# Performance work log

Hardware: AMD Instinct MI355X
Metric: run time of the kernel (lower is better)

Reference implementation:

```python
import math
import jax, jax.numpy as jnp
import numpy as np

D_MODEL = 2048
HEAD = 128
DEPTH = 12
LAMBDA_INIT = 0.8 - 0.6 * math.exp(-0.3 * DEPTH)
RMS_EPS = float(np.finfo(np.float32).eps)  # torch RMSNorm default eps=None -> finfo.eps


def setup_inputs() -> dict:
    key = jax.random.key(0)
    ks = jax.random.split(key, 9)
    B, S = 2, 4096
    std_l = 0.1
    return {
        "x": jax.random.normal(ks[0], (B, S, D_MODEL), dtype=jnp.float32),
        "Wq": jax.random.normal(ks[1], (HEAD, D_MODEL), dtype=jnp.float32) / math.sqrt(D_MODEL),
        "Wk": jax.random.normal(ks[2], (HEAD, D_MODEL), dtype=jnp.float32) / math.sqrt(D_MODEL),
        "Wv": jax.random.normal(ks[3], (HEAD, D_MODEL), dtype=jnp.float32) / math.sqrt(D_MODEL),
        "lambda_q1": std_l * jax.random.normal(ks[4], (HEAD // 2,), dtype=jnp.float32),
        "lambda_q2": std_l * jax.random.normal(ks[5], (HEAD // 2,), dtype=jnp.float32),
        "lambda_k1": std_l * jax.random.normal(ks[6], (HEAD // 2,), dtype=jnp.float32),
        "lambda_k2": std_l * jax.random.normal(ks[7], (HEAD // 2,), dtype=jnp.float32),
        "rms_weight": jnp.ones((HEAD,), dtype=jnp.float32),
    }


def reference(x, Wq, Wk, Wv, lambda_q1, lambda_q2, lambda_k1, lambda_k2, rms_weight):
    # projections (torch Linear: x @ W.T)
    q = jnp.einsum("bsd,hd->bsh", x, Wq)
    k = jnp.einsum("bsd,hd->bsh", x, Wk)
    v = jnp.einsum("bsd,hd->bsh", x, Wv)
    h2 = HEAD // 2
    q1, q2 = q[..., :h2], q[..., h2:]
    k1, k2 = k[..., :h2], k[..., h2:]
    scale = 1.0 / math.sqrt(h2)
    attn1 = jax.nn.softmax(jnp.einsum("bqh,bkh->bqk", q1, k1) * scale, axis=-1)
    attn2 = jax.nn.softmax(jnp.einsum("bqh,bkh->bqk", q2, k2) * scale, axis=-1)
    lam = jnp.exp(jnp.dot(lambda_q1, lambda_k1)) - jnp.exp(jnp.dot(lambda_q2, lambda_k2)) + LAMBDA_INIT
    attn_out = jnp.einsum("bqk,bkh->bqh", attn1 - lam * attn2, v)
    # RMSNorm over last dim
    rms = jax.lax.rsqrt(jnp.mean(attn_out * attn_out, axis=-1, keepdims=True) + RMS_EPS)
    return (1.0 - LAMBDA_INIT) * (attn_out * rms * rms_weight)
```

## Files before the change

kernel.cpp:

```cpp
#include <hip/hip_runtime.h>
#include <hip/hip_bf16.h>
#include <math.h>

#define S_LEN 4096
#define DMODEL 2048
#define HEADD 128

typedef __attribute__((ext_vector_type(8))) short short8;
typedef __attribute__((ext_vector_type(4))) float floatx4;

__device__ __forceinline__ short f2bs(float f) {
  __hip_bfloat16 h = __float2bfloat16(f);
  short s; __builtin_memcpy(&s, &h, 2); return s;
}
__device__ __forceinline__ float bs2f(short s) {
  unsigned u = ((unsigned)(unsigned short)s) << 16;
  float f; __builtin_memcpy(&f, &u, 4); return f;
}
__device__ __forceinline__ int pkbf(float a, float b) {
  return (int)(((unsigned)(unsigned short)f2bs(b) << 16) |
               (unsigned)(unsigned short)f2bs(a));
}
__device__ __forceinline__ float fexp2(float x) { return __builtin_amdgcn_exp2f(x); }

__global__ __launch_bounds__(256) void convw_kernel(const float* __restrict__ wq,
                                                    const float* __restrict__ wk,
                                                    const float* __restrict__ wv,
                                                    short* __restrict__ wc) {
  const int per = 128 * 2048;
  int e = (blockIdx.x * blockDim.x + threadIdx.x) * 4;
  const float* src = (e < per) ? wq : (e < 2 * per) ? wk : wv;
  int off = e & (per - 1);
  float4 v = *(const float4*)(src + off);
  short4 r;
  r.x = f2bs(v.x); r.y = f2bs(v.y); r.z = f2bs(v.z); r.w = f2bs(v.w);
  *(short4*)(wc + e) = r;
}

__global__ __launch_bounds__(256, 3) void proj_kernel(const float* __restrict__ x,
                                                      const short* __restrict__ wc,
                                                      short* __restrict__ qm,
                                                      short* __restrict__ kb,
                                                      short* __restrict__ vstage) {
  const int tid = threadIdx.x;
  const int w = tid >> 6;
  const int lane = tid & 63;
  const int lo = lane & 15, g = lane >> 4;
  const int id = blockIdx.x;
  const int nq = id >> 7, mb = id & 127;
  const int m0 = mb * 64;
  const int n0 = nq * 96;

  __shared__ short xt[2][64 * 64];
  __shared__ short wt[2][96 * 64];

  const int r8 = tid >> 3, sc = tid & 7;
  const float* xs0 = x + (size_t)(m0 + r8) * DMODEL + sc * 8;
  const float* xs1 = x + (size_t)(m0 + 32 + r8) * DMODEL + sc * 8;
  const short* ws0 = wc + (size_t)(n0 + r8) * DMODEL + sc * 8;
  const short* ws1 = wc + (size_t)(n0 + 32 + r8) * DMODEL + sc * 8;
  const short* ws2 = wc + (size_t)(n0 + 64 + r8) * DMODEL + sc * 8;
  const int xl0 = r8 * 64 + ((sc ^ (r8 & 7)) * 8);
  const int xl1 = (32 + r8) * 64 + ((sc ^ (r8 & 7)) * 8);
  const int wlo0 = r8 * 64 + ((sc ^ (r8 & 7)) * 8);
  const int wlo1 = (32 + r8) * 64 + ((sc ^ (r8 & 7)) * 8);
  const int wlo2 = (64 + r8) * 64 + ((sc ^ (r8 & 7)) * 8);

  const int mrow = (w >> 1) * 32;
  const int ncol = (w & 1) * 48;
  int aoff[2][2], boff[3][2];
#pragma unroll
  for (int mi = 0; mi < 2; ++mi) {
    int r = mrow + mi * 16 + lo;
#pragma unroll
    for (int kc = 0; kc < 2; ++kc)
      aoff[mi][kc] = r * 64 + (((kc * 4 + g) ^ (r & 7)) * 8);
  }
#pragma unroll
  for (int t = 0; t < 3; ++t) {
    int r = ncol + t * 16 + lo;
#pragma unroll
    for (int kc = 0; kc < 2; ++kc)
      boff[t][kc] = r * 64 + (((kc * 4 + g) ^ (r & 7)) * 8);
  }

  floatx4 acc[2][3];
#pragma unroll
  for (int mi = 0; mi < 2; ++mi)
#pragma unroll
    for (int t = 0; t < 3; ++t) acc[mi][t] = floatx4{0.f, 0.f, 0.f, 0.f};

  {
    float4 a0 = *(const float4*)(xs0), a1 = *(const float4*)(xs0 + 4);
    float4 b0 = *(const float4*)(xs1), b1 = *(const float4*)(xs1 + 4);
    int4 w0 = *(const int4*)(ws0);
    int4 w1 = *(const int4*)(ws1);
    int4 w2 = *(const int4*)(ws2);
    short8 sA, sB;
    sA[0]=f2bs(a0.x); sA[1]=f2bs(a0.y); sA[2]=f2bs(a0.z); sA[3]=f2bs(a0.w);
    sA[4]=f2bs(a1.x); sA[5]=f2bs(a1.y); sA[6]=f2bs(a1.z); sA[7]=f2bs(a1.w);
    sB[0]=f2bs(b0.x); sB[1]=f2bs(b0.y); sB[2]=f2bs(b0.z); sB[3]=f2bs(b0.w);
    sB[4]=f2bs(b1.x); sB[5]=f2bs(b1.y); sB[6]=f2bs(b1.z); sB[7]=f2bs(b1.w);
    *(short8*)&xt[0][xl0] = sA;
    *(short8*)&xt[0][xl1] = sB;
    *(int4*)&wt[0][wlo0] = w0;
    *(int4*)&wt[0][wlo1] = w1;
    *(int4*)&wt[0][wlo2] = w2;
  }
  __syncthreads();

  int cur = 0;
#pragma unroll 1
  for (int it = 0; it < 32; ++it) {
    float4 a0, a1, b0, b1;
    int4 w0, w1, w2;
    if (it + 1 < 32) {
      const int k = (it + 1) * 64;
      a0 = *(const float4*)(xs0 + k); a1 = *(const float4*)(xs0 + k + 4);
      b0 = *(const float4*)(xs1 + k); b1 = *(const float4*)(xs1 + k + 4);
      w0 = *(const int4*)(ws0 + k);
      w1 = *(const int4*)(ws1 + k);
      w2 = *(const int4*)(ws2 + k);
    }

    {
      const short* xb = &xt[cur][0];
      const short* wb = &wt[cur][0];
      short8 af[2][2], bf[3][2];
#pragma unroll
      for (int mi = 0; mi < 2; ++mi)
#pragma unroll
        for (int kc = 0; kc < 2; ++kc) af[mi][kc] = *(const short8*)(xb + aoff[mi][kc]);
#pragma unroll
      for (int t = 0; t < 3; ++t)
#pragma unroll
        for (int kc = 0; kc < 2; ++kc) bf[t][kc] = *(const short8*)(wb + boff[t][kc]);
#pragma unroll
      for (int kc = 0; kc < 2; ++kc)
#pragma unroll
        for (int mi = 0; mi < 2; ++mi)
#pragma unroll
          for (int t = 0; t < 3; ++t)
            acc[mi][t] = __builtin_amdgcn_mfma_f32_16x16x32_bf16(af[mi][kc], bf[t][kc], acc[mi][t], 0, 0, 0);
    }

    if (it + 1 < 32) {
      short8 sA, sB;
      sA[0]=f2bs(a0.x); sA[1]=f2bs(a0.y); sA[2]=f2bs(a0.z); sA[3]=f2bs(a0.w);
      sA[4]=f2bs(a1.x); sA[5]=f2bs(a1.y); sA[6]=f2bs(a1.z); sA[7]=f2bs(a1.w);
      sB[0]=f2bs(b0.x); sB[1]=f2bs(b0.y); sB[2]=f2bs(b0.z); sB[3]=f2bs(b0.w);
      sB[4]=f2bs(b1.x); sB[5]=f2bs(b1.y); sB[6]=f2bs(b1.z); sB[7]=f2bs(b1.w);
      *(short8*)&xt[cur ^ 1][xl0] = sA;
      *(short8*)&xt[cur ^ 1][xl1] = sB;
      *(int4*)&wt[cur ^ 1][wlo0] = w0;
      *(int4*)&wt[cur ^ 1][wlo1] = w1;
      *(int4*)&wt[cur ^ 1][wlo2] = w2;
    }
    __syncthreads();
    cur ^= 1;
  }

#pragma unroll
  for (int t = 0; t < 3; ++t) {
    int n = n0 + ncol + t * 16 + lo;
#pragma unroll
    for (int mi = 0; mi < 2; ++mi)
#pragma unroll
      for (int j = 0; j < 4; ++j) {
        int m = m0 + mrow + mi * 16 + g * 4 + j;
        float v = acc[mi][t][j];
        if (n < HEADD) {
          qm[(size_t)m * HEADD + n] = f2bs(v * 0.18033688011112042f);
        } else if (n < 2 * HEADD) {
          kb[(size_t)m * HEADD + (n - HEADD)] = f2bs(v);
        } else {
          vstage[(size_t)m * HEADD + (n - 2 * HEADD)] = f2bs(v);
        }
      }
  }
}

__global__ __launch_bounds__(256) void conv_v_kernel(const short* __restrict__ vstage,
                                                     short* __restrict__ vt) {
  const int tid = threadIdx.x;
  const int bb = blockIdx.x >> 6, st = blockIdx.x & 63;
  const int s0 = st * 64;

  __shared__ short ld[64][136];

  const int r = tid >> 2, c8 = (tid & 3) * 32;
#pragma unroll
  for (int q = 0; q < 4; ++q) {
    const size_t off = (size_t)(bb * 4096 + s0 + r) * 128 + c8 + q * 8;
    *(short8*)(&ld[r][c8 + q * 8]) = *(const short8*)(vstage + off);
  }
  __syncthreads();

  const int h = tid >> 1, sh = (tid & 1) * 32;
#pragma unroll
  for (int q = 0; q < 4; ++q) {
    short8 t;
#pragma unroll
    for (int i = 0; i < 8; ++i) t[i] = ld[sh + q * 8 + i][h];
    *(short8*)(vt + ((size_t)bb * 128 + h) * 4096 + s0 + sh + q * 8) = t;
  }
}

__global__ __launch_bounds__(256, 3) void attn_kernel(const short* __restrict__ qm,
                                                      const short* __restrict__ kb,
                                                      const short* __restrict__ vt,
                                                      short* __restrict__ po,
                                                      float* __restrict__ pls) {
  const int tid = threadIdx.x;
  const int w = tid >> 6;
  const int lane = tid & 63;
  const int lo = lane & 15, g = lane >> 4;
  const int qsp = w >> 1;
  const int s = w & 1;
  const int id = blockIdx.x;
  const int ksp = id & 7;
  const int qblk = id >> 3;
  const int b = qblk >> 6;
  const int kv_base = ksp * 512;

  __shared__ short kt[2][32 * 128];
  __shared__ short vl[2][128 * 32];

  const int kr0 = tid >> 4, kck = tid & 15;
  const int vr0 = tid >> 2, vck = tid & 3;
  const short* kS = kb + (size_t)b * S_LEN * HEADD;
  const short* vS = vt + (size_t)b * HEADD * S_LEN;
  const int kld0 = kr0 * 128 + ((kck ^ (kr0 & 7)) * 8);
  const int kld1 = (kr0 + 16) * 128 + ((kck ^ (kr0 & 7)) * 8);
  const int vld0 = vr0 * 32 + ((vck ^ (vr0 & 3)) * 8);
  const int vld1 = (vr0 + 64) * 32 + ((vck ^ (vr0 & 3)) * 8);

  const int rowqA = qblk * 64 + qsp * 32;
  const int rowqB = rowqA + 16;
  const short* qrowA = qm + (size_t)(rowqA + lo) * HEADD + s * 64;
  const short* qrowB = qm + (size_t)(rowqB + lo) * HEADD + s * 64;
  const short8 qA0 = *(const short8*)(qrowA + g * 8);
  const short8 qA1 = *(const short8*)(qrowA + 32 + g * 8);
  const short8 qB0 = *(const short8*)(qrowB + g * 8);
  const short8 qB1 = *(const short8*)(qrowB + 32 + g * 8);

  floatx4 accA[8], accB[8];
#pragma unroll
  for (int n = 0; n < 8; ++n) {
    accA[n] = floatx4{0.f, 0.f, 0.f, 0.f};
    accB[n] = floatx4{0.f, 0.f, 0.f, 0.f};
  }
  float lxA = 0.f, lxB = 0.f;

  const int kc0 = ((s * 8 + g) ^ (lo & 7)) * 8;
  const int kc1 = ((s * 8 + 4 + g) ^ (lo & 7)) * 8;
  const int kro0 = lo * 128, kro1 = (16 + lo) * 128;
  const int vco = (g ^ (lo & 3)) * 8;

  const int gA = (g & 1) * 2;
  const int idx0 = lo + 16 * gA, idx1 = idx0 + 16;
  const bool hi = (g >= 2);

  {
    int4 ka = *(const int4*)(kS + (size_t)(kv_base + kr0) * HEADD + kck * 8);
    int4 kbx = *(const int4*)(kS + (size_t)(kv_base + kr0 + 16) * HEADD + kck * 8);
    int4 va = *(const int4*)(vS + (size_t)vr0 * S_LEN + kv_base + vck * 8);
    int4 vb = *(const int4*)(vS + (size_t)(vr0 + 64) * S_LEN + kv_base + vck * 8);
    *(int4*)(&kt[0][kld0]) = ka;
    *(int4*)(&kt[0][kld1]) = kbx;
    *(int4*)(&vl[0][vld0]) = va;
    *(int4*)(&vl[0][vld1]) = vb;
  }
  __syncthreads();

  int cur = 0;
#pragma unroll 1
  for (int it = 0; it < 16; ++it) {
    int4 ka, kbx, va, vb;
    if (it + 1 < 16) {
      const int kvn = kv_base + (it + 1) * 32;
      ka  = *(const int4*)(kS + (size_t)(kvn + kr0) * HEADD + kck * 8);
      kbx = *(const int4*)(kS + (size_t)(kvn + kr0 + 16) * HEADD + kck * 8);
      va  = *(const int4*)(vS + (size_t)vr0 * S_LEN + kvn + vck * 8);
      vb  = *(const int4*)(vS + (size_t)(vr0 + 64) * S_LEN + kvn + vck * 8);
    }

    const short* kbase = &kt[cur][0];
    short8 a00 = *(const short8*)(kbase + kro0 + kc0);
    short8 a01 = *(const short8*)(kbase + kro0 + kc1);
    short8 a10 = *(const short8*)(kbase + kro1 + kc0);
    short8 a11 = *(const short8*)(kbase + kro1 + kc1);

    floatx4 z = floatx4{0.f, 0.f, 0.f, 0.f};
    floatx4 u;
    u = __builtin_amdgcn_mfma_f32_16x16x32_bf16(a00, qA0, z, 0, 0, 0);
    floatx4 T0A = __builtin_amdgcn_mfma_f32_16x16x32_bf16(a01, qA1, u, 0, 0, 0);
    u = __builtin_amdgcn_mfma_f32_16x16x32_bf16(a10, qA0, z, 0, 0, 0);
    floatx4 T1A = __builtin_amdgcn_mfma_f32_16x16x32_bf16(a11, qA1, u, 0, 0, 0);
    u = __builtin_amdgcn_mfma_f32_16x16x32_bf16(a00, qB0, z, 0, 0, 0);
    floatx4 T0B = __builtin_amdgcn_mfma_f32_16x16x32_bf16(a01, qB1, u, 0, 0, 0);
    u = __builtin_amdgcn_mfma_f32_16x16x32_bf16(a10, qB0, z, 0, 0, 0);
    floatx4 T1B = __builtin_amdgcn_mfma_f32_16x16x32_bf16(a11, qB1, u, 0, 0, 0);

    short8 paA, paB;
    {
      float p0 = fexp2(T0A[0]), p1 = fexp2(T0A[1]), p2 = fexp2(T0A[2]), p3 = fexp2(T0A[3]);
      float p4 = fexp2(T1A[0]), p5 = fexp2(T1A[1]), p6 = fexp2(T1A[2]), p7 = fexp2(T1A[3]);
      float lp = ((p0 + p1) + (p2 + p3)) + ((p4 + p5) + (p6 + p7));
      lp += __shfl_xor(lp, 16);
      lp += __shfl_xor(lp, 32);
      lxA += lp;
      int c00 = pkbf(p0, p1), c01 = pkbf(p2, p3);
      int c10 = pkbf(p4, p5), c11 = pkbf(p6, p7);
      int t0a = __shfl(c00, idx0), t0b = __shfl(c01, idx0);
      int t0c = __shfl(c00, idx1), t0d = __shfl(c01, idx1);
      int t1a = __shfl(c10, idx0), t1b = __shfl(c11, idx0);
      int t1c = __shfl(c10, idx1), t1d = __shfl(c11, idx1);
      int w0 = hi ? t1a : t0a, w1 = hi ? t1b : t0b;
      int w2 = hi ? t1c : t0c, w3 = hi ? t1d : t0d;
      int4 tmp = {w0, w1, w2, w3}; __builtin_memcpy(&paA, &tmp, 16);
    }
    {
      float p0 = fexp2(T0B[0]), p1 = fexp2(T0B[1]), p2 = fexp2(T0B[2]), p3 = fexp2(T0B[3]);
      float p4 = fexp2(T1B[0]), p5 = fexp2(T1B[1]), p6 = fexp2(T1B[2]), p7 = fexp2(T1B[3]);
      float lp = ((p0 + p1) + (p2 + p3)) + ((p4 + p5) + (p6 + p7));
      lp += __shfl_xor(lp, 16);
      lp += __shfl_xor(lp, 32);
      lxB += lp;
      int c00 = pkbf(p0, p1), c01 = pkbf(p2, p3);
      int c10 = pkbf(p4, p5), c11 = pkbf(p6, p7);
      int t0a = __shfl(c00, idx0), t0b = __shfl(c01, idx0);
      int t0c = __shfl(c00, idx1), t0d = __shfl(c01, idx1);
      int t1a = __shfl(c10, idx0), t1b = __shfl(c11, idx0);
      int t1c = __shfl(c10, idx1), t1d = __shfl(c11, idx1);
      int w0 = hi ? t1a : t0a, w1 = hi ? t1b : t0b;
      int w2 = hi ? t1c : t0c, w3 = hi ? t1d : t0d;
      int4 tmp = {w0, w1, w2, w3}; __builtin_memcpy(&paB, &tmp, 16);
    }

    const short* vbase = &vl[cur][0];
#pragma unroll
    for (int n = 0; n < 8; ++n) {
      short8 vf = *(const short8*)(vbase + (n * 16 + lo) * 32 + vco);
      accA[n] = __builtin_amdgcn_mfma_f32_16x16x32_bf16(paA, vf, accA[n], 0, 0, 0);
      accB[n] = __builtin_amdgcn_mfma_f32_16x16x32_bf16(paB, vf, accB[n], 0, 0, 0);
    }

    if (it + 1 < 16) {
      *(int4*)(&kt[cur ^ 1][kld0]) = ka;
      *(int4*)(&kt[cur ^ 1][kld1]) = kbx;
      *(int4*)(&vl[cur ^ 1][vld0]) = va;
      *(int4*)(&vl[cur ^ 1][vld1]) = vb;
    }
    __syncthreads();
    cur ^= 1;
  }

  short* pw = po + ((size_t)(ksp * 2 + s) * 8192) * 128;
#pragma unroll
  for (int j = 0; j < 4; ++j) {
    short8 pk;
#pragma unroll
    for (int n = 0; n < 8; ++n) pk[n] = f2bs(accA[n][j]);
    *(short8*)(pw + (size_t)(rowqA + g * 4 + j) * 128 + lo * 8) = pk;
#pragma unroll
    for (int n = 0; n < 8; ++n) pk[n] = f2bs(accB[n][j]);
    *(short8*)(pw + (size_t)(rowqB + g * 4 + j) * 128 + lo * 8) = pk;
  }
  if (g == 0) {
    pls[(size_t)(ksp * 2 + s) * 8192 + rowqA + lo] = lxA;
    pls[(size_t)(ksp * 2 + s) * 8192 + rowqB + lo] = lxB;
  }
}

__global__ __launch_bounds__(256) void merge_kernel(const short* __restrict__ po,
                                                    const float* __restrict__ pls,
                                                    const float* __restrict__ lq1,
                                                    const float* __restrict__ lq2,
                                                    const float* __restrict__ lk1,
                                                    const float* __restrict__ lk2,
                                                    const float* __restrict__ rmsw,
                                                    float* __restrict__ out) {
  const int tid = threadIdx.x;
  const int row = blockIdx.x * 16 + (tid >> 4);
  const int lo = tid & 15;

  float a1s = 0.f, a2s = 0.f;
  for (int i = 0; i < 64; ++i) {
    a1s = fmaf(lq1[i], lk1[i], a1s);
    a2s = fmaf(lq2[i], lk2[i], a2s);
  }
  const float lam = __expf(a1s) - __expf(a2s) + 0.7836057665316245f;

  float o1[8], o2[8];
#pragma unroll
  for (int n = 0; n < 8; ++n) { o1[n] = 0.f; o2[n] = 0.f; }
  float l1 = 0.f, l2 = 0.f;
#pragma unroll
  for (int ksp = 0; ksp < 8; ++ksp) {
    short8 sa = *(const short8*)(po + ((size_t)(ksp * 2 + 0) * 8192 + row) * 128 + lo * 8);
    short8 sb = *(const short8*)(po + ((size_t)(ksp * 2 + 1) * 8192 + row) * 128 + lo * 8);
#pragma unroll
    for (int n = 0; n < 8; ++n) { o1[n] += bs2f(sa[n]); o2[n] += bs2f(sb[n]); }
    l1 += pls[(size_t)(ksp * 2 + 0) * 8192 + row];
    l2 += pls[(size_t)(ksp * 2 + 1) * 8192 + row];
  }
  const float iL1 = 1.f / l1, iL2 = 1.f / l2;

  float v[8];
  float ssq = 0.f;
#pragma unroll
  for (int n = 0; n < 8; ++n) {
    v[n] = o1[n] * iL1 - lam * (o2[n] * iL2);
    ssq += v[n] * v[n];
  }
  ssq += __shfl_xor(ssq, 1);
  ssq += __shfl_xor(ssq, 2);
  ssq += __shfl_xor(ssq, 4);
  ssq += __shfl_xor(ssq, 8);
  const float rr = rsqrtf(ssq * (1.f / 128.f) + 1.1920928955078125e-07f);

  float* ob = out + (size_t)row * 128;
#pragma unroll
  for (int n = 0; n < 8; ++n) {
    int c = n * 16 + lo;
    ob[c] = 0.21639423346837554f * v[n] * rr * rmsw[c];
  }
}

extern "C" void kernel_launch(void* const* d_in, const int* in_sizes, int n_in,
                              void* d_out, int out_size, void* d_ws, size_t ws_size,
                              hipStream_t stream) {
  const float* x   = (const float*)d_in[0];
  const float* wq  = (const float*)d_in[1];
  const float* wk  = (const float*)d_in[2];
  const float* wv  = (const float*)d_in[3];
  const float* lq1 = (const float*)d_in[4];
  const float* lq2 = (const float*)d_in[5];
  const float* lk1 = (const float*)d_in[6];
  const float* lk2 = (const float*)d_in[7];
  const float* rw  = (const float*)d_in[8];
  float* out = (float*)d_out;

  char* ws = (char*)d_ws;
  short* qm  = (short*)(ws);
  short* kb  = (short*)(ws + (2u << 20));
  short* vt  = (short*)(ws + (4u << 20));
  short* wc  = (short*)(ws + (6u << 20));
  short* vstage = (short*)(ws + (6u << 20) + 1572864u);
  short* po  = (short*)(ws + (8u << 20));
  float* pls = (float*)(ws + (40u << 20));

  convw_kernel<<<768, 256, 0, stream>>>(wq, wk, wv, wc);
  proj_kernel<<<512, 256, 0, stream>>>(x, wc, qm, kb, vstage);
  conv_v_kernel<<<128, 256, 0, stream>>>(vstage, vt);
  attn_kernel<<<1024, 256, 0, stream>>>(qm, kb, vt, po, pls);
  merge_kernel<<<512, 256, 0, stream>>>(po, pls, lq1, lq2, lk1, lk2, rw, out);
}
```

Measured before the change: 96.64 us.

## Permute V transpose layout so P fragments feed MFMA without lane shuffles

Reorders the key positions in the transposed V staging so the bf16 P values each lane already holds from the QK^T MFMA line up with the B-operand layout of the PV MFMA. This removes eight cross-lane shuffles and selects per P tile in the attention inner loop. The gain depends on the permuted V write in the transpose kernel matching the MFMA register layout exactly; the transpose now reads LDS rows in a non-contiguous pattern.

```diff
diff --git a/kernel.cpp b/kernel.cpp
--- a/kernel.cpp
+++ b/kernel.cpp
@@ -201,7 +201,10 @@
   for (int q = 0; q < 4; ++q) {
     short8 t;
 #pragma unroll
-    for (int i = 0; i < 8; ++i) t[i] = ld[sh + q * 8 + i][h];
+    for (int i = 0; i < 8; ++i) {
+      int src5 = (i < 4) ? (4 * q + i) : (16 + 4 * q + (i - 4));
+      t[i] = ld[sh + src5][h];
+    }
     *(short8*)(vt + ((size_t)bb * 128 + h) * 4096 + s0 + sh + q * 8) = t;
   }
 }
@@ -257,10 +260,6 @@
   const int kro0 = lo * 128, kro1 = (16 + lo) * 128;
   const int vco = (g ^ (lo & 3)) * 8;
 
-  const int gA = (g & 1) * 2;
-  const int idx0 = lo + 16 * gA, idx1 = idx0 + 16;
-  const bool hi = (g >= 2);
-
   {
     int4 ka = *(const int4*)(kS + (size_t)(kv_base + kr0) * HEADD + kck * 8);
     int4 kbx = *(const int4*)(kS + (size_t)(kv_base + kr0 + 16) * HEADD + kck * 8);
@@ -310,15 +309,8 @@
       lp += __shfl_xor(lp, 16);
       lp += __shfl_xor(lp, 32);
       lxA += lp;
-      int c00 = pkbf(p0, p1), c01 = pkbf(p2, p3);
-      int c10 = pkbf(p4, p5), c11 = pkbf(p6, p7);
-      int t0a = __shfl(c00, idx0), t0b = __shfl(c01, idx0);
-      int t0c = __shfl(c00, idx1), t0d = __shfl(c01, idx1);
-      int t1a = __shfl(c10, idx0), t1b = __shfl(c11, idx0);
-      int t1c = __shfl(c10, idx1), t1d = __shfl(c11, idx1);
-      int w0 = hi ? t1a : t0a, w1 = hi ? t1b : t0b;
-      int w2 = hi ? t1c : t0c, w3 = hi ? t1d : t0d;
-      int4 tmp = {w0, w1, w2, w3}; __builtin_memcpy(&paA, &tmp, 16);
+      int4 tmp = {pkbf(p0, p1), pkbf(p2, p3), pkbf(p4, p5), pkbf(p6, p7)};
+      __builtin_memcpy(&paA, &tmp, 16);
     }
     {
       float p0 = fexp2(T0B[0]), p1 = fexp2(T0B[1]), p2 = fexp2(T0B[2]), p3 = fexp2(T0B[3]);
@@ -327,15 +319,8 @@
       lp += __shfl_xor(lp, 16);
       lp += __shfl_xor(lp, 32);
       lxB += lp;
-      int c00 = pkbf(p0, p1), c01 = pkbf(p2, p3);
-      int c10 = pkbf(p4, p5), c11 = pkbf(p6, p7);
-      int t0a = __shfl(c00, idx0), t0b = __shfl(c01, idx0);
-      int t0c = __shfl(c00, idx1), t0d = __shfl(c01, idx1);
-      int t1a = __shfl(c10, idx0), t1b = __shfl(c11, idx0);
-      int t1c = __shfl(c10, idx1), t1d = __shfl(c11, idx1);
-      int w0 = hi ? t1a : t0a, w1 = hi ? t1b : t0b;
-      int w2 = hi ? t1c : t0c, w3 = hi ? t1d : t0d;
-      int4 tmp = {w0, w1, w2, w3}; __builtin_memcpy(&paB, &tmp, 16);
+      int4 tmp = {pkbf(p0, p1), pkbf(p2, p3), pkbf(p4, p5), pkbf(p6, p7)};
+      __builtin_memcpy(&paB, &tmp, 16);
     }
 
     const short* vbase = &vl[cur][0];
```

Result: faster. 92.73 us (-4.0%).
